# Optimization experiments

Hardware: AMD Instinct MI355X
Metric: run time of the kernel (lower is better)

## Reference

```python
import jax, jax.numpy as jnp
import numpy as np

D, H = 1024, 2048
N_STEPS = 2
T0, T1 = 0.0, 1.0


def setup_inputs() -> dict:
    key = jax.random.key(0)
    ks = jax.random.split(key, 5)
    s_in = 1.0 / np.sqrt(D)
    s_h = 1.0 / np.sqrt(H)
    return {
        "x0": jax.random.normal(ks[0], (D,), jnp.float32),
        "W1": jax.random.normal(ks[1], (D, H), jnp.float32) * s_in,
        "b1": jnp.zeros((H,), jnp.float32),
        "wt": jax.random.normal(ks[2], (H,), jnp.float32) * 0.1,
        "W2": jax.random.normal(ks[3], (H, H), jnp.float32) * s_h,
        "b2": jnp.zeros((H,), jnp.float32),
        "W3": jax.random.normal(ks[4], (H, D), jnp.float32) * s_h,
        "b3": jnp.zeros((D,), jnp.float32),
    }


def reference(x0, W1, b1, wt, W2, b2, W3, b3):
    dtype = x0.dtype

    def velocity(t, x):
        # 3-layer tanh MLP velocity field with additive time embedding
        h1 = jnp.tanh(x @ W1 + b1 + t * wt)
        h2 = jnp.tanh(h1 @ W2 + b2)
        return h2 @ W3 + b3

    def vel_and_div(t, x):
        # Mirror of _compute_velocity_and_divergence: linearize + vmap(jvp)
        # over identity to get the full Jacobian, then take its trace.
        v, jvp_fun = jax.linearize(lambda z: velocity(t, z), x)
        cols = jax.vmap(jvp_fun)(jnp.eye(D, dtype=dtype))  # [D, D]
        return v, jnp.trace(cols)

    def aug_dyn(t, x):
        v, div = vel_and_div(t, x)
        return v, -div  # (dx/dt, dlogq/dt)

    # Standard-normal base distribution log_prob at x0
    log2pi = jnp.log(jnp.asarray(2.0 * np.pi, dtype=dtype))
    logq0 = -0.5 * jnp.sum(x0 * x0) - 0.5 * D * log2pi

    dt = jnp.asarray((T1 - T0) / N_STEPS, dtype=dtype)

    def rk4_step(carry, i):
        x, logq = carry
        t = T0 + i * dt
        v1, dl1 = aug_dyn(t, x)
        v2, dl2 = aug_dyn(t + 0.5 * dt, x + 0.5 * dt * v1)
        v3, dl3 = aug_dyn(t + 0.5 * dt, x + 0.5 * dt * v2)
        v4, dl4 = aug_dyn(t + dt, x + dt * v3)
        x_new = x + (dt / 6.0) * (v1 + 2.0 * v2 + 2.0 * v3 + v4)
        logq_new = logq + (dt / 6.0) * (dl1 + 2.0 * dl2 + 2.0 * dl3 + dl4)
        return (x_new, logq_new), None

    (x1, logq1), _ = jax.lax.scan(
        rk4_step, (x0, logq0), jnp.arange(N_STEPS, dtype=dtype)
    )
    # concat [x1 (D,), logq1 ()] -> (D+1,) for a single output array
    return jnp.concatenate([x1, logq1[None]])
```

## Files before the change

### kernel.cpp

```cpp
#include <hip/hip_runtime.h>
#include <math.h>

#define DD 1024
#define HH 2048
#define NCB 256

typedef float f32x4 __attribute__((ext_vector_type(4)));
typedef short short8 __attribute__((ext_vector_type(8)));

__device__ __forceinline__ float b2f(unsigned short u) {
    return __uint_as_float(((unsigned int)u) << 16);
}
__device__ __forceinline__ unsigned short f2b(float f) {
    unsigned int x = __float_as_uint(f);
    unsigned int r = (x + 0x7FFFu + ((x >> 16) & 1u)) >> 16;
    return (unsigned short)r;
}
__device__ __forceinline__ float ald(const float* p) {
    return __hip_atomic_load(p, __ATOMIC_RELAXED, __HIP_MEMORY_SCOPE_AGENT);
}
__device__ __forceinline__ void ast(float* p, float v) {
    __hip_atomic_store(p, v, __ATOMIC_RELAXED, __HIP_MEMORY_SCOPE_AGENT);
}

__global__ __launch_bounds__(256) void k_gemmPT(const float* __restrict__ W1,
                                                const float* __restrict__ W2,
                                                const float* __restrict__ W3,
                                                const float* __restrict__ b3,
                                                const float* __restrict__ x0,
                                                unsigned short* __restrict__ Mb,
                                                unsigned short* __restrict__ Pb,
                                                unsigned short* __restrict__ W2T,
                                                unsigned short* __restrict__ W3T,
                                                float* __restrict__ c1,
                                                float* __restrict__ A1g,
                                                unsigned* __restrict__ sync) {
    const int b = blockIdx.x, t = threadIdx.x;
    if (b >= 256) {
        int bb = b - 256;
        if (bb == 0) {
            #pragma unroll
            for (int q = 0; q < 18; ++q) {
                int i = t + q * 256;
                if (i < 4368) sync[i] = 0u;
            }
        }
        __shared__ float tile[64][65];
        const float* in; unsigned short* out; int R, C, bx, by;
        if (bb < 1024) { in = W2; out = W2T; R = HH; C = HH; bx = bb & 31; by = bb >> 5; }
        else           { bb -= 1024; in = W3; out = W3T; R = HH; C = DD; bx = bb & 15; by = bb >> 4; }
        const int c0 = bx * 64, r0 = by * 64;
        const int cc = t & 63, rb = t >> 6;
        #pragma unroll
        for (int p = 0; p < 16; ++p) {
            int rr = p * 4 + rb;
            tile[rr][cc] = in[(size_t)(r0 + rr) * C + c0 + cc];
        }
        __syncthreads();
        #pragma unroll
        for (int p = 0; p < 16; ++p) {
            int rr = p * 4 + rb;
            out[(size_t)(c0 + rr) * R + r0 + cc] = f2b(tile[cc][rr]);
        }
        return;
    }
    __shared__ unsigned short At[128][40];
    __shared__ unsigned short Bt[128][40];
    const int m0 = (b & 15) * 128;
    const int k0 = (b >> 4) * 128;
    const int r = t & 127, half = t >> 7;
    const int wv = t >> 6, l = t & 63;
    const int wr = wv >> 1, wc = wv & 1;
    const int fr = l & 15, fg = l >> 4;
    const bool do_aux = ((b >> 4) == 0) && (t < 128);
    float c1acc = 0.f, a1acc = 0.f;

    f32x4 acc[4][4] = {};
    for (int i0 = 0; i0 < DD; i0 += 32) {
        {
            const float* wp = W1 + (size_t)(i0 + half * 16) * HH + m0 + r;
            float v[16];
            #pragma unroll
            for (int k2 = 0; k2 < 16; ++k2) v[k2] = wp[(size_t)k2 * HH];
            short8 o0, o1;
            #pragma unroll
            for (int e = 0; e < 8; ++e) { o0[e] = (short)f2b(v[e]); o1[e] = (short)f2b(v[8 + e]); }
            *(short8*)&At[r][half * 16] = o0;
            *(short8*)&At[r][half * 16 + 8] = o1;
        }
        {
            const float4* sbf = (const float4*)(W3 + (size_t)(k0 + r) * DD + i0 + half * 16);
            float4 f0 = sbf[0], f1 = sbf[1], f2v = sbf[2], f3 = sbf[3];
            short8 o0, o1;
            o0[0] = (short)f2b(f0.x); o0[1] = (short)f2b(f0.y); o0[2] = (short)f2b(f0.z); o0[3] = (short)f2b(f0.w);
            o0[4] = (short)f2b(f1.x); o0[5] = (short)f2b(f1.y); o0[6] = (short)f2b(f1.z); o0[7] = (short)f2b(f1.w);
            o1[0] = (short)f2b(f2v.x); o1[1] = (short)f2b(f2v.y); o1[2] = (short)f2b(f2v.z); o1[3] = (short)f2b(f2v.w);
            o1[4] = (short)f2b(f3.x); o1[5] = (short)f2b(f3.y); o1[6] = (short)f2b(f3.z); o1[7] = (short)f2b(f3.w);
            *(short8*)&Bt[r][half * 16] = o0;
            *(short8*)&Bt[r][half * 16 + 8] = o1;
        }
        __syncthreads();
        if (do_aux) {
            #pragma unroll
            for (int i = 0; i < 32; ++i) {
                float w1v = b2f(At[t][i]);
                c1acc += w1v * b3[i0 + i];
                a1acc += w1v * x0[i0 + i];
            }
        }
        short8 af[4], bf[4];
        #pragma unroll
        for (int a = 0; a < 4; ++a)
            af[a] = *(const short8*)&At[wr * 64 + a * 16 + fr][fg * 8];
        #pragma unroll
        for (int bq = 0; bq < 4; ++bq)
            bf[bq] = *(const short8*)&Bt[wc * 64 + bq * 16 + fr][fg * 8];
        #pragma unroll
        for (int a = 0; a < 4; ++a)
            #pragma unroll
            for (int bq = 0; bq < 4; ++bq)
                acc[a][bq] = __builtin_amdgcn_mfma_f32_16x16x32_bf16(af[a], bf[bq], acc[a][bq], 0, 0, 0);
        __syncthreads();
    }
    if (do_aux) { c1[m0 + t] = c1acc; A1g[m0 + t] = a1acc; }
    #pragma unroll
    for (int a = 0; a < 4; ++a) {
        #pragma unroll
        for (int bq = 0; bq < 4; ++bq) {
            #pragma unroll
            for (int j = 0; j < 4; ++j) {
                int row = m0 + wr * 64 + a * 16 + fg * 4 + j;
                int col = k0 + wc * 64 + bq * 16 + fr;
                size_t idx = (size_t)row * HH + col;
                float m = acc[a][bq][j];
                Mb[idx] = f2b(m);
                Pb[idx] = f2b(m * W2[idx]);
            }
        }
    }
}

__device__ __forceinline__ void gbar(unsigned* sync, int b, unsigned g) {
    __syncthreads();
    if (threadIdx.x < 64) {
        if (threadIdx.x == 0) {
            asm volatile("s_waitcnt vmcnt(0)" ::: "memory");
            __hip_atomic_store(&sync[b << 4], g, __ATOMIC_RELAXED, __HIP_MEMORY_SCOPE_AGENT);
        }
        while (true) {
            bool ok = true;
            #pragma unroll
            for (int k = 0; k < 4; ++k) {
                unsigned f = __hip_atomic_load(&sync[(threadIdx.x + (k << 6)) << 4],
                                               __ATOMIC_RELAXED, __HIP_MEMORY_SCOPE_AGENT);
                ok &= (f >= g);
            }
            if (!__any((int)(!ok))) break;
            __builtin_amdgcn_s_sleep(1);
        }
    }
    __syncthreads();
}

__global__ __launch_bounds__(256, 1) void k_chain(
    const unsigned short* __restrict__ Mb,
    const unsigned short* __restrict__ Pb,
    const unsigned short* __restrict__ W2T,
    const unsigned short* __restrict__ W3T,
    const float* __restrict__ x0,
    const float* __restrict__ b1, const float* __restrict__ wt,
    const float* __restrict__ b2, const float* __restrict__ b3,
    const float* __restrict__ c1, const float* __restrict__ A1g,
    float* __restrict__ h1_g, float* __restrict__ h2_g, float* __restrict__ hacc_g,
    float* __restrict__ out,
    unsigned* __restrict__ sync) {
    __shared__ unsigned short Ms[8][2048];
    __shared__ unsigned short Ps[8][2048];
    __shared__ unsigned short Qs[8][2048];
    __shared__ float vecH[2048];
    __shared__ float vecW[2048];
    __shared__ float wred[4];
    const int t = threadIdx.x, b = blockIdx.x;
    const int wib = t >> 6, lane = t & 63;
    const int gw2 = (b << 3) + (wib << 1);
    const int jx = (b << 2) + wib;
    unsigned g = 0;

    {
        const unsigned short* mp = Mb + (size_t)gw2 * HH;
        const unsigned short* pp = Pb + (size_t)gw2 * HH;
        const unsigned short* qp = W2T + (size_t)gw2 * HH;
        #pragma unroll
        for (int rep = 0; rep < 4; ++rep) {
            const int idx = rep * 512 + lane * 8;
            *(short8*)&Ms[wib * 2][idx]     = *(const short8*)(mp + idx);
            *(short8*)&Ms[wib * 2 + 1][idx] = *(const short8*)(mp + HH + idx);
            *(short8*)&Ps[wib * 2][idx]     = *(const short8*)(pp + idx);
            *(short8*)&Ps[wib * 2 + 1][idx] = *(const short8*)(pp + HH + idx);
            *(short8*)&Qs[wib * 2][idx]     = *(const short8*)(qp + idx);
            *(short8*)&Qs[wib * 2 + 1][idx] = *(const short8*)(qp + HH + idx);
        }
    }

    const float bb1_0 = b1[gw2], bb1_1 = b1[gw2 + 1];
    const float wt_0 = wt[gw2], wt_1 = wt[gw2 + 1];
    const float bb2_0 = b2[gw2], bb2_1 = b2[gw2 + 1];
    const float c1_0 = c1[gw2], c1_1 = c1[gw2 + 1];

    float A1_0 = 0.f, A1_1 = 0.f;
    float u0 = 0.f, u1 = 0.f;
    float hc0 = 0.f, hc1 = 0.f;
    float wdiv = 0.f;

    float logq_r = 0.f;
    if (b == 0 && wib == 0) {
        float ssum = 0.f;
        #pragma unroll
        for (int q = 0; q < 16; ++q) { float xv = x0[lane + (q << 6)]; ssum += xv * xv; }
        #pragma unroll
        for (int o = 1; o < 64; o <<= 1) ssum += __shfl_xor(ssum, o, 64);
        logq_r = -0.5f * ssum - 0.5f * 1024.0f * 1.8378770664093453f;
    }

    for (int s = 0; s < 8; ++s) {
        const int ss = s & 3;
        const float tcur = (s >> 2) * 0.5f + ((ss == 0) ? 0.f : (ss == 3) ? 0.5f : 0.25f);

        if (s == 0) {
            A1_0 = A1g[gw2]; A1_1 = A1g[gw2 + 1];
            float h0 = tanhf(A1_0 + bb1_0 + tcur * wt_0);
            float h1v = tanhf(A1_1 + bb1_1 + tcur * wt_1);
            u0 = 1.f - h0 * h0; u1 = 1.f - h1v * h1v;
            if (lane == 0) { ast(h1_g + gw2, h0); ast(h1_g + gw2 + 1, h1v); }
        } else {
            #pragma unroll
            for (int q = 0; q < 8; ++q) {
                int i = t + (q << 8);
                float h2v = ald(h2_g + i);
                float sv = (ss == 0) ? ald(hacc_g + i) : h2v;
                vecH[i] = sv;
                vecW[i] = 1.f - h2v * h2v;
            }
            __syncthreads();
            float md0 = 0.f, md1 = 0.f, pd0 = 0.f, pd1 = 0.f;
            #pragma unroll
            for (int rep = 0; rep < 4; ++rep) {
                const int idx = rep * 512 + lane * 8;
                float4 hA = *(const float4*)(vecH + idx);
                float4 hB = *(const float4*)(vecH + idx + 4);
                float4 wA = *(const float4*)(vecW + idx);
                float4 wB = *(const float4*)(vecW + idx + 4);
                float hv[8] = {hA.x, hA.y, hA.z, hA.w, hB.x, hB.y, hB.z, hB.w};
                float wv[8] = {wA.x, wA.y, wA.z, wA.w, wB.x, wB.y, wB.z, wB.w};
                short8 m0v = *(const short8*)&Ms[wib * 2][idx];
                short8 m1v = *(const short8*)&Ms[wib * 2 + 1][idx];
                short8 p0v = *(const short8*)&Ps[wib * 2][idx];
                short8 p1v = *(const short8*)&Ps[wib * 2 + 1][idx];
                #pragma unroll
                for (int e = 0; e < 8; ++e) {
                    md0 += b2f((unsigned short)m0v[e]) * hv[e];
                    md1 += b2f((unsigned short)m1v[e]) * hv[e];
                    pd0 += b2f((unsigned short)p0v[e]) * wv[e];
                    pd1 += b2f((unsigned short)p1v[e]) * wv[e];
                }
            }
            #pragma unroll
            for (int o = 1; o < 64; o <<= 1) {
                md0 += __shfl_xor(md0, o, 64); md1 += __shfl_xor(md1, o, 64);
                pd0 += __shfl_xor(pd0, o, 64); pd1 += __shfl_xor(pd1, o, 64);
            }
            const int sp = (s - 1) & 3;
            const float cprev = (sp == 1 || sp == 2) ? (1.f / 6.f) : (1.f / 12.f);
            wdiv += cprev * (u0 * pd0 + u1 * pd1);
            float pre0, pre1;
            if (ss == 0) {
                A1_0 += md0 + 0.5f * c1_0; A1_1 += md1 + 0.5f * c1_1;
                pre0 = A1_0 + bb1_0 + tcur * wt_0; pre1 = A1_1 + bb1_1 + tcur * wt_1;
            } else {
                const float a = (ss == 3) ? 0.5f : 0.25f;
                pre0 = A1_0 + a * (md0 + c1_0) + bb1_0 + tcur * wt_0;
                pre1 = A1_1 + a * (md1 + c1_1) + bb1_1 + tcur * wt_1;
            }
            float h0 = tanhf(pre0), h1v = tanhf(pre1);
            u0 = 1.f - h0 * h0; u1 = 1.f - h1v * h1v;
            if (lane == 0) { ast(h1_g + gw2, h0); ast(h1_g + gw2 + 1, h1v); }
        }
        gbar(sync, b, ++g);

        #pragma unroll
        for (int q = 0; q < 8; ++q) {
            int i = t + (q << 8);
            vecH[i] = ald(h1_g + i);
        }
        __syncthreads();
        {
            float a0 = 0.f, a1 = 0.f;
            #pragma unroll
            for (int rep = 0; rep < 4; ++rep) {
                const int idx = rep * 512 + lane * 8;
                float4 hA = *(const float4*)(vecH + idx);
                float4 hB = *(const float4*)(vecH + idx + 4);
                float hv[8] = {hA.x, hA.y, hA.z, hA.w, hB.x, hB.y, hB.z, hB.w};
                short8 r0 = *(const short8*)&Qs[wib * 2][idx];
                short8 r1 = *(const short8*)&Qs[wib * 2 + 1][idx];
                #pragma unroll
                for (int e = 0; e < 8; ++e) {
                    a0 += b2f((unsigned short)r0[e]) * hv[e];
                    a1 += b2f((unsigned short)r1[e]) * hv[e];
                }
            }
            #pragma unroll
            for (int o = 1; o < 64; o <<= 1) {
                a0 += __shfl_xor(a0, o, 64); a1 += __shfl_xor(a1, o, 64);
            }
            float q0 = tanhf(a0 + bb2_0), q1 = tanhf(a1 + bb2_1);
            const float cs = (ss == 1 || ss == 2) ? (1.f / 6.f) : (1.f / 12.f);
            hc0 += cs * q0; hc1 += cs * q1;
            if (lane == 0) {
                ast(h2_g + gw2, q0); ast(h2_g + gw2 + 1, q1);
                if (ss == 3) { ast(hacc_g + gw2, hc0); ast(hacc_g + gw2 + 1, hc1); }
            }
        }
        gbar(sync, b, ++g);
    }

    {
        #pragma unroll
        for (int q = 0; q < 8; ++q) {
            int i = t + (q << 8);
            float h2v = ald(h2_g + i);
            vecH[i] = ald(hacc_g + i);
            vecW[i] = 1.f - h2v * h2v;
        }
        __syncthreads();
        float pd0 = 0.f, pd1 = 0.f, xo = 0.f;
        const unsigned short* Vr = W3T + (size_t)jx * HH;
        #pragma unroll
        for (int rep = 0; rep < 4; ++rep) {
            const int idx = rep * 512 + lane * 8;
            float4 cA = *(const float4*)(vecH + idx);
            float4 cB = *(const float4*)(vecH + idx + 4);
            float4 wA = *(const float4*)(vecW + idx);
            float4 wB = *(const float4*)(vecW + idx + 4);
            float cv[8] = {cA.x, cA.y, cA.z, cA.w, cB.x, cB.y, cB.z, cB.w};
            float wv[8] = {wA.x, wA.y, wA.z, wA.w, wB.x, wB.y, wB.z, wB.w};
            short8 p0v = *(const short8*)&Ps[wib * 2][idx];
            short8 p1v = *(const short8*)&Ps[wib * 2 + 1][idx];
            short8 vv = *(const short8*)(Vr + idx);
            #pragma unroll
            for (int e = 0; e < 8; ++e) {
                pd0 += b2f((unsigned short)p0v[e]) * wv[e];
                pd1 += b2f((unsigned short)p1v[e]) * wv[e];
                xo  += b2f((unsigned short)vv[e]) * cv[e];
            }
        }
        #pragma unroll
        for (int o = 1; o < 64; o <<= 1) {
            pd0 += __shfl_xor(pd0, o, 64); pd1 += __shfl_xor(pd1, o, 64);
            xo += __shfl_xor(xo, o, 64);
        }
        wdiv += (1.f / 12.f) * (u0 * pd0 + u1 * pd1);
        if (lane == 0) {
            out[jx] = x0[jx] + xo + b3[jx];
            wred[wib] = wdiv;
        }
    }
    __syncthreads();
    if (t == 0) {
        float dsum = wred[0] + wred[1] + wred[2] + wred[3];
        atomicAdd((float*)(sync + 4096 + (b & 15) * 16), dsum);
        asm volatile("s_waitcnt vmcnt(0)" ::: "memory");
        atomicAdd(sync + 4352, 1u);
    }
    if (b == 0 && wib == 0) {
        if (lane == 0) {
            while (__hip_atomic_load(sync + 4352, __ATOMIC_RELAXED, __HIP_MEMORY_SCOPE_AGENT) < NCB)
                __builtin_amdgcn_s_sleep(2);
        }
        float v = 0.f;
        if (lane < 16) {
            unsigned du = __hip_atomic_load(sync + 4096 + lane * 16,
                                            __ATOMIC_RELAXED, __HIP_MEMORY_SCOPE_AGENT);
            v = __uint_as_float(du);
        }
        #pragma unroll
        for (int o = 1; o < 64; o <<= 1) v += __shfl_xor(v, o, 64);
        if (lane == 0) out[DD] = logq_r - v;
    }
}

extern "C" void kernel_launch(void* const* d_in, const int* in_sizes, int n_in,
                              void* d_out, int out_size, void* d_ws, size_t ws_size,
                              hipStream_t stream) {
    const float* x0 = (const float*)d_in[0];
    const float* W1 = (const float*)d_in[1];
    const float* b1 = (const float*)d_in[2];
    const float* wt = (const float*)d_in[3];
    const float* W2 = (const float*)d_in[4];
    const float* b2 = (const float*)d_in[5];
    const float* W3 = (const float*)d_in[6];
    const float* b3 = (const float*)d_in[7];
    float* out = (float*)d_out;

    char* ws = (char*)d_ws;
    const size_t MB = 1024 * 1024;
    unsigned short* Pb  = (unsigned short*)(ws);
    unsigned short* W2T = (unsigned short*)(ws + 8 * MB);
    unsigned short* W3T = (unsigned short*)(ws + 16 * MB);
    unsigned short* Mb  = (unsigned short*)(ws + 20 * MB);
    float* fb = (float*)(ws + 28 * MB);
    float* c1      = fb;
    float* A1g     = fb + 2048;
    float* h1_g    = fb + 4096;
    float* h2_g    = fb + 6144;
    float* hacc_g  = fb + 8192;
    unsigned* sync = (unsigned*)(fb + 10240);

    k_gemmPT<<<1792, 256, 0, stream>>>(W1, W2, W3, b3, x0, Mb, Pb, W2T, W3T,
                                       c1, A1g, sync);
    k_chain<<<NCB, 256, 0, stream>>>(Mb, Pb, W2T, W3T, x0, b1, wt, b2, b3, c1, A1g,
                                     h1_g, h2_g, hacc_g, out, sync);
}
```

Before: 173.5 us.

## Pre-transpose W1 to bf16 in separate kernel before the P GEMM

Adds W1 to the transpose kernel, writing a bf16 transposed W1T, and splits the former fused GEMM+transpose launch into two kernels. The GEMM then loads W1T rows with contiguous vector loads instead of strided per-column fp32 loads plus conversion. This removes uncoalesced W1 reads from the GEMM, but adds an extra kernel launch, an extra pass over W1, and serializes the transposes before the GEMM where they previously ran concurrently in one grid.

```diff
diff --git a/kernel.cpp b/kernel.cpp
--- a/kernel.cpp
+++ b/kernel.cpp
@@ -23,49 +23,53 @@
     __hip_atomic_store(p, v, __ATOMIC_RELAXED, __HIP_MEMORY_SCOPE_AGENT);
 }
 
-__global__ __launch_bounds__(256) void k_gemmPT(const float* __restrict__ W1,
-                                                const float* __restrict__ W2,
-                                                const float* __restrict__ W3,
-                                                const float* __restrict__ b3,
-                                                const float* __restrict__ x0,
-                                                unsigned short* __restrict__ Mb,
-                                                unsigned short* __restrict__ Pb,
-                                                unsigned short* __restrict__ W2T,
-                                                unsigned short* __restrict__ W3T,
-                                                float* __restrict__ c1,
-                                                float* __restrict__ A1g,
-                                                unsigned* __restrict__ sync) {
+__global__ __launch_bounds__(256) void k_tr(const float* __restrict__ W1,
+                                            const float* __restrict__ W2,
+                                            const float* __restrict__ W3,
+                                            unsigned short* __restrict__ W1T,
+                                            unsigned short* __restrict__ W2T,
+                                            unsigned short* __restrict__ W3T,
+                                            unsigned* __restrict__ sync) {
+    __shared__ float tile[64][65];
     const int b = blockIdx.x, t = threadIdx.x;
-    if (b >= 256) {
-        int bb = b - 256;
-        if (bb == 0) {
-            #pragma unroll
-            for (int q = 0; q < 18; ++q) {
-                int i = t + q * 256;
-                if (i < 4368) sync[i] = 0u;
-            }
-        }
-        __shared__ float tile[64][65];
-        const float* in; unsigned short* out; int R, C, bx, by;
-        if (bb < 1024) { in = W2; out = W2T; R = HH; C = HH; bx = bb & 31; by = bb >> 5; }
-        else           { bb -= 1024; in = W3; out = W3T; R = HH; C = DD; bx = bb & 15; by = bb >> 4; }
-        const int c0 = bx * 64, r0 = by * 64;
-        const int cc = t & 63, rb = t >> 6;
-        #pragma unroll
-        for (int p = 0; p < 16; ++p) {
-            int rr = p * 4 + rb;
-            tile[rr][cc] = in[(size_t)(r0 + rr) * C + c0 + cc];
-        }
-        __syncthreads();
-        #pragma unroll
-        for (int p = 0; p < 16; ++p) {
-            int rr = p * 4 + rb;
-            out[(size_t)(c0 + rr) * R + r0 + cc] = f2b(tile[cc][rr]);
-        }
-        return;
-    }
+    if (b == 0) {
+        #pragma unroll
+        for (int q = 0; q < 18; ++q) {
+            int i = t + q * 256;
+            if (i < 4368) sync[i] = 0u;
+        }
+    }
+    const float* in; unsigned short* out; int R, C, bx, by;
+    if (b < 512)       { int bb = b;        in = W1; out = W1T; R = DD; C = HH; bx = bb & 31; by = bb >> 5; }
+    else if (b < 1536) { int bb = b - 512;  in = W2; out = W2T; R = HH; C = HH; bx = bb & 31; by = bb >> 5; }
+    else               { int bb = b - 1536; in = W3; out = W3T; R = HH; C = DD; bx = bb & 15; by = bb >> 4; }
+    const int c0 = bx * 64, r0 = by * 64;
+    const int cc = t & 63, rb = t >> 6;
+    #pragma unroll
+    for (int p = 0; p < 16; ++p) {
+        int rr = p * 4 + rb;
+        tile[rr][cc] = in[(size_t)(r0 + rr) * C + c0 + cc];
+    }
+    __syncthreads();
+    #pragma unroll
+    for (int p = 0; p < 16; ++p) {
+        int rr = p * 4 + rb;
+        out[(size_t)(c0 + rr) * R + r0 + cc] = f2b(tile[cc][rr]);
+    }
+}
+
+__global__ __launch_bounds__(256) void k_gemmP(const unsigned short* __restrict__ W1T,
+                                               const float* __restrict__ W3,
+                                               const float* __restrict__ W2,
+                                               const float* __restrict__ b3,
+                                               const float* __restrict__ x0,
+                                               unsigned short* __restrict__ Mb,
+                                               unsigned short* __restrict__ Pb,
+                                               float* __restrict__ c1,
+                                               float* __restrict__ A1g) {
     __shared__ unsigned short At[128][40];
     __shared__ unsigned short Bt[128][40];
+    const int b = blockIdx.x, t = threadIdx.x;
     const int m0 = (b & 15) * 128;
     const int k0 = (b >> 4) * 128;
     const int r = t & 127, half = t >> 7;
@@ -78,15 +82,10 @@
     f32x4 acc[4][4] = {};
     for (int i0 = 0; i0 < DD; i0 += 32) {
         {
-            const float* wp = W1 + (size_t)(i0 + half * 16) * HH + m0 + r;
-            float v[16];
-            #pragma unroll
-            for (int k2 = 0; k2 < 16; ++k2) v[k2] = wp[(size_t)k2 * HH];
-            short8 o0, o1;
-            #pragma unroll
-            for (int e = 0; e < 8; ++e) { o0[e] = (short)f2b(v[e]); o1[e] = (short)f2b(v[8 + e]); }
-            *(short8*)&At[r][half * 16] = o0;
-            *(short8*)&At[r][half * 16 + 8] = o1;
+            const float4* sa = (const float4*)(W1T + (size_t)(m0 + r) * DD + i0 + half * 16);
+            float4 a0 = sa[0], a1 = sa[1];
+            float4* da = (float4*)&At[r][half * 16];
+            da[0] = a0; da[1] = a1;
         }
         {
             const float4* sbf = (const float4*)(W3 + (size_t)(k0 + r) * DD + i0 + half * 16);
@@ -408,7 +407,8 @@
     unsigned short* W2T = (unsigned short*)(ws + 8 * MB);
     unsigned short* W3T = (unsigned short*)(ws + 16 * MB);
     unsigned short* Mb  = (unsigned short*)(ws + 20 * MB);
-    float* fb = (float*)(ws + 28 * MB);
+    unsigned short* W1T = (unsigned short*)(ws + 28 * MB);
+    float* fb = (float*)(ws + 32 * MB);
     float* c1      = fb;
     float* A1g     = fb + 2048;
     float* h1_g    = fb + 4096;
@@ -416,8 +416,8 @@
     float* hacc_g  = fb + 8192;
     unsigned* sync = (unsigned*)(fb + 10240);
 
-    k_gemmPT<<<1792, 256, 0, stream>>>(W1, W2, W3, b3, x0, Mb, Pb, W2T, W3T,
-                                       c1, A1g, sync);
+    k_tr<<<2048, 256, 0, stream>>>(W1, W2, W3, W1T, W2T, W3T, sync);
+    k_gemmP<<<256, 256, 0, stream>>>(W1T, W3, W2, b3, x0, Mb, Pb, c1, A1g);
     k_chain<<<NCB, 256, 0, stream>>>(Mb, Pb, W2T, W3T, x0, b1, wt, b2, b3, c1, A1g,
                                      h1_g, h2_g, hacc_g, out, sync);
 }
```

Result: faster. 169.3 us (-2.4%).
